# Kernel optimization log

Measured on AMD Instinct MI355X. Metric: run time of the kernel, lower is better.

## Reference

```python
import jax, jax.numpy as jnp
import numpy as np

B, T, IN_DIM, LATENT = 32, 8192, 6, 256
EPS = 1e-5


def _build_chain_edge_index(b, t):
    self_idx = np.arange(t)
    idx = np.arange(t - 1)
    src = np.concatenate([self_idx, idx, idx + 1])
    dst = np.concatenate([self_idx, idx + 1, idx])
    ei = np.stack([src, dst], axis=0)  # [2, t + 2(t-1)]
    batched = np.concatenate([ei + i * t for i in range(b)], axis=1)
    return jnp.asarray(batched, dtype=jnp.int32)


def setup_inputs() -> dict:
    key = jax.random.key(0)
    ks = jax.random.split(key, 16)
    p = lambda k, shape, s=0.1: jax.random.normal(k, shape, jnp.float32) * s
    return {
        "x": jax.random.normal(ks[0], (B, T, IN_DIM), jnp.float32),
        "ei": _build_chain_edge_index(B, T),
        "W1": p(ks[1], (IN_DIM, 12)), "b1": jnp.zeros((12,), jnp.float32),
        "W2": p(ks[2], (12, 12)), "b2": jnp.zeros((12,), jnp.float32),
        "W3": p(ks[3], (12, 24)), "b3": jnp.zeros((24,), jnp.float32),
        "g1": jnp.ones((12,), jnp.float32), "be1": jnp.zeros((12,), jnp.float32),
        "g2": jnp.ones((12,), jnp.float32), "be2": jnp.zeros((12,), jnp.float32),
        "g3": jnp.ones((24,), jnp.float32), "be3": jnp.zeros((24,), jnp.float32),
        "Wo": p(ks[4], (24, LATENT)), "bo": jnp.zeros((LATENT,), jnp.float32),
    }


def _gcn_conv(h, src, dst, n, W, b):
    # PyG GCNConv, add_self_loops=False: out[dst] += d^-1/2[src] d^-1/2[dst] * (h W)[src]; + bias
    hw = h @ W
    deg = jax.ops.segment_sum(jnp.ones(src.shape[0], h.dtype), dst, num_segments=n)
    dinv = jnp.where(deg > 0, jax.lax.rsqrt(jnp.maximum(deg, 1.0)), 0.0)
    norm = dinv[src] * dinv[dst]  # [E]
    agg = jax.ops.segment_sum(hw[src] * norm[:, None], dst, num_segments=n)
    return agg + b


def _layernorm(x, g, b):
    mu = jnp.mean(x, axis=-1, keepdims=True)
    var = jnp.mean(jnp.square(x - mu), axis=-1, keepdims=True)
    return (x - mu) * jax.lax.rsqrt(var + EPS) * g + b


def reference(x, ei, W1, b1, W2, b2, W3, b3, g1, be1, g2, be2, g3, be3, Wo, bo):
    b, t, _ = x.shape
    n = b * t
    src, dst = ei[0], ei[1]
    h = x.reshape(n, -1)
    # dropout layers are identity in eval mode
    h = jax.nn.relu(_layernorm(_gcn_conv(h, src, dst, n, W1, b1), g1, be1))
    h = jax.nn.relu(_layernorm(_gcn_conv(h, src, dst, n, W2, b2), g2, be2))
    h = jax.nn.relu(_layernorm(_gcn_conv(h, src, dst, n, W3, b3), g3, be3))
    return (h @ Wo + bo).reshape(b, t, -1)
```

## Files before the change

kernel.cpp:

```cpp
#include <hip/hip_runtime.h>
#include <hip/hip_bf16.h>

constexpr int Bb = 32, Tt = 8192;
constexpr int Nn = Bb * Tt;
constexpr float EPS = 1e-5f;

constexpr float DINV3 = 0.57735026918962576f;
constexpr float DINV2 = 0.70710678118654752f;

constexpr int TILE = 250;
constexpr int NT = (Tt + TILE - 1) / TILE;

#define DEVI __device__ __forceinline__

template <int DIN, int DOUT, int LAYER>
DEVI void gcn_layer(float* h, float* S, int tid, int p, bool inchain, float dinv,
                    const float* __restrict__ W,
                    const float* __restrict__ bias,
                    const float* __restrict__ g,
                    const float* __restrict__ be)
{
    float hw[DOUT];
#pragma unroll
    for (int j = 0; j < DOUT; j++) {
        float acc = 0.f;
#pragma unroll
        for (int k = 0; k < DIN; k++)
            acc += h[k] * W[k * DOUT + j];
        hw[j] = acc;
    }
#pragma unroll
    for (int j = 0; j < DOUT; j++)
        S[tid * 25 + j] = inchain ? hw[j] * dinv : 0.f;
    __syncthreads();

    if (tid >= LAYER && tid < 256 - LAYER && inchain) {
        float v[DOUT];
        float mu = 0.f;
#pragma unroll
        for (int j = 0; j < DOUT; j++) {
            float s = S[tid * 25 + j];
            if (p > 0)      s += S[(tid - 1) * 25 + j];
            if (p < Tt - 1) s += S[(tid + 1) * 25 + j];
            v[j] = dinv * s + bias[j];
            mu += v[j];
        }
        mu *= (1.0f / DOUT);
        float var = 0.f;
#pragma unroll
        for (int j = 0; j < DOUT; j++) { float d = v[j] - mu; var += d * d; }
        var *= (1.0f / DOUT);
        float rstd = rsqrtf(var + EPS);
#pragma unroll
        for (int j = 0; j < DOUT; j++) {
            float y = (v[j] - mu) * rstd * g[j] + be[j];
            h[j] = y > 0.f ? y : 0.f;
        }
    }
    __syncthreads();
}

__global__ __launch_bounds__(256) void gcn_fused(
    const float* __restrict__ x,
    const float* __restrict__ W1, const float* __restrict__ b1,
    const float* __restrict__ W2, const float* __restrict__ b2,
    const float* __restrict__ W3, const float* __restrict__ b3,
    const float* __restrict__ g1, const float* __restrict__ be1,
    const float* __restrict__ g2, const float* __restrict__ be2,
    const float* __restrict__ g3, const float* __restrict__ be3,
    float* __restrict__ h3out)
{
    __shared__ float S[256 * 25];
    const int tid = threadIdx.x;
    const int b = blockIdx.x / NT;
    const int tile = blockIdx.x % NT;
    const int p = tile * TILE + tid - 3;
    const bool inchain = (p >= 0 && p < Tt);
    const float dinv = (p == 0 || p == Tt - 1) ? DINV2 : DINV3;
    const size_t node = (size_t)b * Tt + (size_t)(p < 0 ? 0 : p);

    float h[24];
#pragma unroll
    for (int k = 0; k < 24; k++) h[k] = 0.f;
    if (inchain) {
#pragma unroll
        for (int k = 0; k < 6; k++)
            h[k] = x[node * 6 + k];
    }

    gcn_layer<6, 12, 1>(h, S, tid, p, inchain, dinv, W1, b1, g1, be1);
    gcn_layer<12, 12, 2>(h, S, tid, p, inchain, dinv, W2, b2, g2, be2);
    gcn_layer<12, 24, 3>(h, S, tid, p, inchain, dinv, W3, b3, g3, be3);

    if (tid >= 3 && tid < 253 && inchain) {
        float4* o = reinterpret_cast<float4*>(h3out + node * 24);
#pragma unroll
        for (int q = 0; q < 6; q++) {
            float4 v;
            v.x = h[q * 4 + 0]; v.y = h[q * 4 + 1];
            v.z = h[q * 4 + 2]; v.w = h[q * 4 + 3];
            o[q] = v;
        }
    }
}

__global__ __launch_bounds__(256) void proj_kernel(
    const float* __restrict__ h3,
    const float* __restrict__ Wo,
    const float* __restrict__ bo,
    float* __restrict__ out)
{
    __shared__ float WoS[24 * 256];
    __shared__ float boS[256];
    __shared__ float hS[64 * 24];

    const int tid = threadIdx.x;
    {
        const float4* src = reinterpret_cast<const float4*>(Wo);
        float4* dst = reinterpret_cast<float4*>(WoS);
#pragma unroll
        for (int q = 0; q < 6; q++) dst[tid + 256 * q] = src[tid + 256 * q];
    }
    boS[tid] = bo[tid];
    const size_t nbase = (size_t)blockIdx.x * 64;
    {
        const float4* src = reinterpret_cast<const float4*>(h3 + nbase * 24);
        float4* dst = reinterpret_cast<float4*>(hS);
        for (int i = tid; i < 384; i += 256)
            dst[i] = src[i];
    }
    __syncthreads();

    const int cx = tid & 31;
    const int ny = tid >> 5;

    float acc[8][8];
#pragma unroll
    for (int i = 0; i < 8; i++)
#pragma unroll
        for (int m = 0; m < 8; m++) acc[i][m] = boS[cx + 32 * m];

#pragma unroll
    for (int k = 0; k < 24; k++) {
        float w[8], hv[8];
#pragma unroll
        for (int m = 0; m < 8; m++) w[m] = WoS[k * 256 + cx + 32 * m];
#pragma unroll
        for (int i = 0; i < 8; i++) hv[i] = hS[(ny * 8 + i) * 24 + k];
#pragma unroll
        for (int i = 0; i < 8; i++)
#pragma unroll
            for (int m = 0; m < 8; m++) acc[i][m] += hv[i] * w[m];
    }

#pragma unroll
    for (int i = 0; i < 8; i++) {
        const size_t n = nbase + (size_t)(ny * 8 + i);
#pragma unroll
        for (int m = 0; m < 8; m++)
            out[n * 256 + cx + 32 * m] = acc[i][m];
    }
}

extern "C" void kernel_launch(void* const* d_in, const int* in_sizes, int n_in,
                              void* d_out, int out_size, void* d_ws, size_t ws_size,
                              hipStream_t stream) {
    const float* x   = (const float*)d_in[0];
    const float* W1  = (const float*)d_in[2];
    const float* b1  = (const float*)d_in[3];
    const float* W2  = (const float*)d_in[4];
    const float* b2  = (const float*)d_in[5];
    const float* W3  = (const float*)d_in[6];
    const float* b3  = (const float*)d_in[7];
    const float* g1  = (const float*)d_in[8];
    const float* be1 = (const float*)d_in[9];
    const float* g2  = (const float*)d_in[10];
    const float* be2 = (const float*)d_in[11];
    const float* g3  = (const float*)d_in[12];
    const float* be3 = (const float*)d_in[13];
    const float* Wo  = (const float*)d_in[14];
    const float* bo  = (const float*)d_in[15];

    float* h3 = (float*)d_ws;

    gcn_fused<<<Bb * NT, 256, 0, stream>>>(
        x, W1, b1, W2, b2, W3, b3, g1, be1, g2, be2, g3, be3, h3);

    proj_kernel<<<Nn / 64, 256, 0, stream>>>(
        h3, Wo, bo, (float*)d_out);
}
```

Before: 344.6 us.

## Fuse output projection into GCN kernel and drop intermediate h3 buffer

```diff
diff --git a/kernel.cpp b/kernel.cpp
--- a/kernel.cpp
+++ b/kernel.cpp
@@ -1,8 +1,6 @@
 #include <hip/hip_runtime.h>
-#include <hip/hip_bf16.h>
 
 constexpr int Bb = 32, Tt = 8192;
-constexpr int Nn = Bb * Tt;
 constexpr float EPS = 1e-5f;
 
 constexpr float DINV3 = 0.57735026918962576f;
@@ -12,6 +10,8 @@
 constexpr int NT = (Tt + TILE - 1) / TILE;
 
 #define DEVI __device__ __forceinline__
+
+using f32x4 = __attribute__((ext_vector_type(4))) float;
 
 template <int DIN, int DOUT, int LAYER>
 DEVI void gcn_layer(float* h, float* S, int tid, int p, bool inchain, float dinv,
@@ -60,7 +60,15 @@
     __syncthreads();
 }
 
-__global__ __launch_bounds__(256) void gcn_fused(
+DEVI float4 f4fma(float a, const float4& b, float4 c) {
+    c.x = fmaf(a, b.x, c.x);
+    c.y = fmaf(a, b.y, c.y);
+    c.z = fmaf(a, b.z, c.z);
+    c.w = fmaf(a, b.w, c.w);
+    return c;
+}
+
+__global__ __launch_bounds__(256) void gcn_proj_fused(
     const float* __restrict__ x,
     const float* __restrict__ W1, const float* __restrict__ b1,
     const float* __restrict__ W2, const float* __restrict__ b2,
@@ -68,10 +76,22 @@
     const float* __restrict__ g1, const float* __restrict__ be1,
     const float* __restrict__ g2, const float* __restrict__ be2,
     const float* __restrict__ g3, const float* __restrict__ be3,
-    float* __restrict__ h3out)
+    const float* __restrict__ Wo, const float* __restrict__ bo,
+    float* __restrict__ out)
 {
-    __shared__ float S[256 * 25];
+    __shared__ float4 SU4[1792];
+    __shared__ float4 WoS4[1536];
+    float* S = reinterpret_cast<float*>(SU4);
+
     const int tid = threadIdx.x;
+
+    {
+        const float4* src = reinterpret_cast<const float4*>(Wo);
+#pragma unroll
+        for (int q = 0; q < 6; q++)
+            WoS4[tid + 256 * q] = src[tid + 256 * q];
+    }
+
     const int b = blockIdx.x / NT;
     const int tile = blockIdx.x % NT;
     const int p = tile * TILE + tid - 3;
@@ -92,73 +112,53 @@
     gcn_layer<12, 12, 2>(h, S, tid, p, inchain, dinv, W2, b2, g2, be2);
     gcn_layer<12, 24, 3>(h, S, tid, p, inchain, dinv, W3, b3, g3, be3);
 
-    if (tid >= 3 && tid < 253 && inchain) {
-        float4* o = reinterpret_cast<float4*>(h3out + node * 24);
+    if (tid >= 3 && tid < 253) {
+        const int idx = tid - 3;
 #pragma unroll
-        for (int q = 0; q < 6; q++) {
-            float4 v;
-            v.x = h[q * 4 + 0]; v.y = h[q * 4 + 1];
-            v.z = h[q * 4 + 2]; v.w = h[q * 4 + 3];
-            o[q] = v;
-        }
-    }
-}
-
-__global__ __launch_bounds__(256) void proj_kernel(
-    const float* __restrict__ h3,
-    const float* __restrict__ Wo,
-    const float* __restrict__ bo,
-    float* __restrict__ out)
-{
-    __shared__ float WoS[24 * 256];
-    __shared__ float boS[256];
-    __shared__ float hS[64 * 24];
-
-    const int tid = threadIdx.x;
-    {
-        const float4* src = reinterpret_cast<const float4*>(Wo);
-        float4* dst = reinterpret_cast<float4*>(WoS);
-#pragma unroll
-        for (int q = 0; q < 6; q++) dst[tid + 256 * q] = src[tid + 256 * q];
-    }
-    boS[tid] = bo[tid];
-    const size_t nbase = (size_t)blockIdx.x * 64;
-    {
-        const float4* src = reinterpret_cast<const float4*>(h3 + nbase * 24);
-        float4* dst = reinterpret_cast<float4*>(hS);
-        for (int i = tid; i < 384; i += 256)
-            dst[i] = src[i];
+        for (int q = 0; q < 6; q++)
+            SU4[idx * 7 + q] = make_float4(h[4 * q + 0], h[4 * q + 1],
+                                           h[4 * q + 2], h[4 * q + 3]);
     }
     __syncthreads();
 
-    const int cx = tid & 31;
-    const int ny = tid >> 5;
+    const int c4q = tid & 63;
+    const int gq  = tid >> 6;
+    const float4 bo4 = reinterpret_cast<const float4*>(bo)[c4q];
+    f32x4* out4 = reinterpret_cast<f32x4*>(out);
+    const size_t nrow = (size_t)b * Tt;
+    const int tb = tile * TILE;
 
-    float acc[8][8];
+    for (int ibl = 0; ibl < 4; ibl++) {
+        float4 acc[16];
 #pragma unroll
-    for (int i = 0; i < 8; i++)
-#pragma unroll
-        for (int m = 0; m < 8; m++) acc[i][m] = boS[cx + 32 * m];
+        for (int ii = 0; ii < 16; ii++) acc[ii] = bo4;
 
 #pragma unroll
-    for (int k = 0; k < 24; k++) {
-        float w[8], hv[8];
+        for (int k4 = 0; k4 < 6; k4++) {
+            const float4 w0 = WoS4[(k4 * 4 + 0) * 64 + c4q];
+            const float4 w1 = WoS4[(k4 * 4 + 1) * 64 + c4q];
+            const float4 w2 = WoS4[(k4 * 4 + 2) * 64 + c4q];
+            const float4 w3 = WoS4[(k4 * 4 + 3) * 64 + c4q];
 #pragma unroll
-        for (int m = 0; m < 8; m++) w[m] = WoS[k * 256 + cx + 32 * m];
-#pragma unroll
-        for (int i = 0; i < 8; i++) hv[i] = hS[(ny * 8 + i) * 24 + k];
-#pragma unroll
-        for (int i = 0; i < 8; i++)
-#pragma unroll
-            for (int m = 0; m < 8; m++) acc[i][m] += hv[i] * w[m];
-    }
+            for (int ii = 0; ii < 16; ii++) {
+                const int idx = (ibl * 16 + ii) * 4 + gq;
+                const float4 hv = SU4[idx * 7 + k4];
+                acc[ii] = f4fma(hv.x, w0, acc[ii]);
+                acc[ii] = f4fma(hv.y, w1, acc[ii]);
+                acc[ii] = f4fma(hv.z, w2, acc[ii]);
+                acc[ii] = f4fma(hv.w, w3, acc[ii]);
+            }
+        }
 
 #pragma unroll
-    for (int i = 0; i < 8; i++) {
-        const size_t n = nbase + (size_t)(ny * 8 + i);
-#pragma unroll
-        for (int m = 0; m < 8; m++)
-            out[n * 256 + cx + 32 * m] = acc[i][m];
+        for (int ii = 0; ii < 16; ii++) {
+            const int idx = (ibl * 16 + ii) * 4 + gq;
+            const int pp = tb + idx;
+            if (idx < TILE && pp < Tt) {
+                f32x4 v; v.x = acc[ii].x; v.y = acc[ii].y; v.z = acc[ii].z; v.w = acc[ii].w;
+                __builtin_nontemporal_store(v, &out4[(nrow + pp) * 64 + c4q]);
+            }
+        }
     }
 }
 
@@ -181,11 +181,7 @@
     const float* Wo  = (const float*)d_in[14];
     const float* bo  = (const float*)d_in[15];
 
-    float* h3 = (float*)d_ws;
-
-    gcn_fused<<<Bb * NT, 256, 0, stream>>>(
-        x, W1, b1, W2, b2, W3, b3, g1, be1, g2, be2, g3, be3, h3);
-
-    proj_kernel<<<Nn / 64, 256, 0, stream>>>(
-        h3, Wo, bo, (float*)d_out);
+    gcn_proj_fused<<<Bb * NT, 256, 0, stream>>>(
+        x, W1, b1, W2, b2, W3, b3, g1, be1, g2, be2, g3, be3, Wo, bo,
+        (float*)d_out);
 }
```

After: 378.1 us. 9.7% more time.
